# Optimization experiments

Measured on AMD Instinct MI355X. Metric: run time of the kernel, lower is better.

Reference implementation:

```python
import jax, jax.numpy as jnp
import numpy as np

B, N, H = 8, 256, 128
EDGE_IN = 2 * H + 1
NODE_IN = 2 * H


def _glorot(key, shape):
    fan_in, fan_out = shape[0], shape[1]
    lim = 1.0 / np.sqrt(fan_in)
    return jax.random.uniform(key, shape, jnp.float32, -lim, lim)


def setup_inputs() -> dict:
    key = jax.random.key(0)
    ks = jax.random.split(key, 12)
    node_state = jax.random.normal(ks[0], (B, N, H), jnp.float32)
    positions = jax.random.normal(ks[1], (B, N, 3), jnp.float32)
    mask = jnp.ones((B, N), jnp.float32)
    # edge_mlp: Linear(2H+1 -> H), SiLU, Linear(H -> H)  (weights stored [in, out])
    We1 = _glorot(ks[2], (EDGE_IN, H)); be1 = _glorot(ks[3], (1, H))[0]
    We2 = _glorot(ks[4], (H, H));       be2 = _glorot(ks[5], (1, H))[0]
    # node_mlp: Linear(2H -> H), SiLU, Linear(H -> H)
    Wn1 = _glorot(ks[6], (NODE_IN, H)); bn1 = _glorot(ks[7], (1, H))[0]
    Wn2 = _glorot(ks[8], (H, H));       bn2 = _glorot(ks[9], (1, H))[0]
    return {"node_state": node_state, "positions": positions, "mask": mask,
            "We1": We1, "be1": be1, "We2": We2, "be2": be2,
            "Wn1": Wn1, "bn1": bn1, "Wn2": Wn2, "bn2": bn2}


def reference(node_state, positions, mask, We1, be1, We2, be2, Wn1, bn1, Wn2, bn2):
    b, n, h = node_state.shape
    # pairwise distances [B, N, N, 1]; safe-sqrt so grad at i==j is 0 (exact fwd)
    rel = positions[:, :, None, :] - positions[:, None, :, :]
    sq = jnp.sum(rel * rel, axis=-1, keepdims=True)
    dist = jnp.where(sq > 0, jnp.sqrt(jnp.where(sq > 0, sq, 1.0)), 0.0)
    # broadcast-concat node features for all pairs -> [B, N, N, 2H+1]
    node_i = jnp.broadcast_to(node_state[:, :, None, :], (b, n, n, h))
    node_j = jnp.broadcast_to(node_state[:, None, :, :], (b, n, n, h))
    edge_input = jnp.concatenate([node_i, node_j, dist], axis=-1)
    edge_msg = jax.nn.silu(edge_input @ We1 + be1) @ We2 + be2  # [B,N,N,H]
    # pairwise validity mask [B, N, N, 1]
    edge_mask = (mask[:, None, :] * mask[:, :, None])[..., None]
    edge_msg = edge_msg * edge_mask
    # masked mean over j
    denom = jnp.clip(jnp.sum(edge_mask, axis=2), 1.0, None)  # [B,N,1]
    aggregated = jnp.sum(edge_msg, axis=2) / denom           # [B,N,H]
    node_in = jnp.concatenate([node_state, aggregated], axis=-1)
    updated = jax.nn.silu(node_in @ Wn1 + bn1) @ Wn2 + bn2
    return node_state + updated * mask[..., None]
```

## Files before the change

kernel.cpp:

```cpp
#include <hip/hip_runtime.h>
#include <hip/hip_bf16.h>
#include <math.h>

#define B_ 8
#define N_ 256
#define H_ 128
#define NODES_ (B_ * N_)

__device__ __forceinline__ float silu_fast(float x) {
    float e = __expf(-x);
    return x * __builtin_amdgcn_rcpf(1.0f + e);
}

__global__ __launch_bounds__(512) void k1(
    const float* __restrict__ node, const float* __restrict__ We1,
    const float* __restrict__ be1, const float* __restrict__ Wn1,
    const float* __restrict__ bn1, const float* __restrict__ mask,
    float* __restrict__ P, float* __restrict__ Q, float* __restrict__ pre)
{
    __shared__ float act[4][128];
    __shared__ float pls[16][4][128];
    const int t = threadIdx.x;
    const int g = blockIdx.x >> 9;
    const int node0 = (blockIdx.x & 511) * 4;

    if (t < 128) {
        int r = t >> 5, col = (t & 31) * 4;
        *(float4*)(&act[r][col]) = *(const float4*)(node + (size_t)(node0 + r) * H_ + col);
    }
    const float* W = (g == 0) ? We1 : (g == 1) ? (We1 + 128 * H_) : Wn1;
    const int kseg = t >> 5;
    const int c0   = (t & 31) * 4;
    __syncthreads();

    float4 w[8];
    const float* Wb = W + (size_t)(kseg * 8) * H_ + c0;
    #pragma unroll
    for (int u = 0; u < 8; ++u) w[u] = *(const float4*)(Wb + u * H_);

    #pragma unroll
    for (int n = 0; n < 4; ++n) {
        float4 a = {0.f, 0.f, 0.f, 0.f};
        #pragma unroll
        for (int u = 0; u < 8; ++u) {
            float v = act[n][kseg * 8 + u];
            a.x = fmaf(v, w[u].x, a.x);
            a.y = fmaf(v, w[u].y, a.y);
            a.z = fmaf(v, w[u].z, a.z);
            a.w = fmaf(v, w[u].w, a.w);
        }
        *(float4*)(&pls[kseg][n][c0]) = a;
    }
    __syncthreads();

    {
        const int n = t >> 7;
        const int c = t & 127;
        float s = 0.f;
        #pragma unroll
        for (int seg = 0; seg < 16; ++seg) s += pls[seg][n][c];
        float* op;
        if (g == 0)      { op = P;   s += be1[c]; }
        else if (g == 1) { op = Q;   s += (mask[node0 + n] - 1.0f) * 1e30f; }
        else             { op = pre; s += bn1[c]; }
        op[(size_t)(node0 + n) * H_ + c] = s;
    }
}

__global__ __launch_bounds__(512) void k2bc(
    const float* __restrict__ P, const float* __restrict__ Q,
    const float* __restrict__ We1, const float* __restrict__ positions,
    const float* __restrict__ mask, const float* __restrict__ pre,
    const float* __restrict__ node,
    const float* __restrict__ We2, const float* __restrict__ be2,
    const float* __restrict__ Wn1, const float* __restrict__ Wn2,
    const float* __restrict__ bn2, float* __restrict__ out)
{
    __shared__ float arena[8192];
    __shared__ float dls[256][4];
    __shared__ float Sls[4][128];
    __shared__ float Tls[4][128];
    __shared__ float cs;
    const int t  = threadIdx.x;
    const int b  = blockIdx.x >> 6;
    const int i0 = (blockIdx.x & 63) * 4;

    {
        const int t2 = t & 255;
        const int half = t >> 8;
        const int il = t2 & 3;
        const int jb = t2 >> 2;
        const float* pb = positions + b * N_ * 3;
        const float pix = pb[(i0 + il) * 3 + 0];
        const float piy = pb[(i0 + il) * 3 + 1];
        const float piz = pb[(i0 + il) * 3 + 2];
        #pragma unroll
        for (int s = 0; s < 2; ++s) {
            int j = jb + 64 * (half * 2 + s);
            float dx = pix - pb[j * 3 + 0];
            float dy = piy - pb[j * 3 + 1];
            float dz = piz - pb[j * 3 + 2];
            float sq = dx * dx + dy * dy + dz * dz;
            dls[j][il] = (sq > 0.f) ? sqrtf(sq) : 0.f;
        }
    }
    if (t < 64) {
        float mv = mask[b * N_ + t] + mask[b * N_ + 64 + t]
                 + mask[b * N_ + 128 + t] + mask[b * N_ + 192 + t];
        #pragma unroll
        for (int off = 32; off >= 1; off >>= 1) mv += __shfl_down(mv, off);
        if (t == 0) cs = mv;
    }

    const int i = t >> 7;
    const int c = t & 127;
    const float wd   = We1[256 * H_ + c];
    const float base = P[(size_t)(b * N_ + i0 + i) * H_ + c];
    const float4* __restrict__ Qg = (const float4*)(Q + (size_t)(b * N_) * H_);

    float4 r0 = Qg[0 * 512 + t];
    float4 r1 = Qg[1 * 512 + t];
    float4 r2 = Qg[2 * 512 + t];
    float4 r3 = Qg[3 * 512 + t];

    float acc = 0.f;
    for (int ch = 0; ch < 4; ++ch) {
        __syncthreads();
        ((float4*)arena)[0 * 512 + t] = r0;
        ((float4*)arena)[1 * 512 + t] = r1;
        ((float4*)arena)[2 * 512 + t] = r2;
        ((float4*)arena)[3 * 512 + t] = r3;
        if (ch < 3) {
            r0 = Qg[(ch + 1) * 2048 + 0 * 512 + t];
            r1 = Qg[(ch + 1) * 2048 + 1 * 512 + t];
            r2 = Qg[(ch + 1) * 2048 + 2 * 512 + t];
            r3 = Qg[(ch + 1) * 2048 + 3 * 512 + t];
        }
        __syncthreads();
        const int j0 = ch * 64;
        #pragma unroll 8
        for (int jj = 0; jj < 64; ++jj) {
            float q = arena[jj * 128 + c];
            float d = dls[j0 + jj][i];
            float x = fmaf(d, wd, base + q);
            float e = __expf(-x);
            float r = __builtin_amdgcn_rcpf(1.0f + e);
            acc = fmaf(x, r, acc);
        }
    }

    const float inv_cnt = __builtin_amdgcn_rcpf(fmaxf(cs, 1.0f));
    const float mi = mask[b * N_ + i0 + i];
    Sls[i][c] = (mi * inv_cnt) * acc;
    __syncthreads();

    float (*pls)[4][128] = (float (*)[4][128])arena;
    const int kseg = t >> 5;
    const int c0   = (t & 31) * 4;

    {
        const float* Wb = We2 + (size_t)(kseg * 8) * H_ + c0;
        float4 w[8];
        #pragma unroll
        for (int u = 0; u < 8; ++u) w[u] = *(const float4*)(Wb + u * H_);
        #pragma unroll
        for (int n = 0; n < 4; ++n) {
            float4 a = {0.f, 0.f, 0.f, 0.f};
            #pragma unroll
            for (int u = 0; u < 8; ++u) {
                float v = Sls[n][kseg * 8 + u];
                a.x = fmaf(v, w[u].x, a.x); a.y = fmaf(v, w[u].y, a.y);
                a.z = fmaf(v, w[u].z, a.z); a.w = fmaf(v, w[u].w, a.w);
            }
            *(float4*)(&pls[kseg][n][c0]) = a;
        }
    }
    __syncthreads();
    {
        float s = 0.f;
        #pragma unroll
        for (int seg = 0; seg < 16; ++seg) s += pls[seg][i][c];
        Tls[i][c] = fmaf(mi, be2[c], s);
    }
    __syncthreads();

    {
        const float* Wb = Wn1 + (size_t)(128 + kseg * 8) * H_ + c0;
        float4 w[8];
        #pragma unroll
        for (int u = 0; u < 8; ++u) w[u] = *(const float4*)(Wb + u * H_);
        #pragma unroll
        for (int n = 0; n < 4; ++n) {
            float4 a = {0.f, 0.f, 0.f, 0.f};
            #pragma unroll
            for (int u = 0; u < 8; ++u) {
                float v = Tls[n][kseg * 8 + u];
                a.x = fmaf(v, w[u].x, a.x); a.y = fmaf(v, w[u].y, a.y);
                a.z = fmaf(v, w[u].z, a.z); a.w = fmaf(v, w[u].w, a.w);
            }
            *(float4*)(&pls[kseg][n][c0]) = a;
        }
    }
    __syncthreads();
    {
        float s = 0.f;
        #pragma unroll
        for (int seg = 0; seg < 16; ++seg) s += pls[seg][i][c];
        float h = silu_fast(pre[(size_t)(b * N_ + i0 + i) * H_ + c] + s);
        Sls[i][c] = h;
    }
    __syncthreads();

    {
        const float* Wb = Wn2 + (size_t)(kseg * 8) * H_ + c0;
        float4 w[8];
        #pragma unroll
        for (int u = 0; u < 8; ++u) w[u] = *(const float4*)(Wb + u * H_);
        #pragma unroll
        for (int n = 0; n < 4; ++n) {
            float4 a = {0.f, 0.f, 0.f, 0.f};
            #pragma unroll
            for (int u = 0; u < 8; ++u) {
                float v = Sls[n][kseg * 8 + u];
                a.x = fmaf(v, w[u].x, a.x); a.y = fmaf(v, w[u].y, a.y);
                a.z = fmaf(v, w[u].z, a.z); a.w = fmaf(v, w[u].w, a.w);
            }
            *(float4*)(&pls[kseg][n][c0]) = a;
        }
    }
    __syncthreads();
    {
        float s = 0.f;
        #pragma unroll
        for (int seg = 0; seg < 16; ++seg) s += pls[seg][i][c];
        const size_t idx = (size_t)(b * N_ + i0 + i) * H_ + c;
        out[idx] = node[idx] + mi * (s + bn2[c]);
    }
}

extern "C" void kernel_launch(void* const* d_in, const int* in_sizes, int n_in,
                              void* d_out, int out_size, void* d_ws, size_t ws_size,
                              hipStream_t stream)
{
    const float* node      = (const float*)d_in[0];
    const float* positions = (const float*)d_in[1];
    const float* mask      = (const float*)d_in[2];
    const float* We1       = (const float*)d_in[3];
    const float* be1       = (const float*)d_in[4];
    const float* We2       = (const float*)d_in[5];
    const float* be2       = (const float*)d_in[6];
    const float* Wn1       = (const float*)d_in[7];
    const float* bn1       = (const float*)d_in[8];
    const float* Wn2       = (const float*)d_in[9];
    const float* bn2       = (const float*)d_in[10];
    float* out = (float*)d_out;

    const size_t SZ = (size_t)NODES_ * H_;
    float* P   = (float*)d_ws;
    float* Q   = P + SZ;
    float* pre = Q + SZ;

    k1  <<<1536, 512, 0, stream>>>(node, We1, be1, Wn1, bn1, mask, P, Q, pre);
    k2bc<<<512,  512, 0, stream>>>(P, Q, We1, positions, mask, pre, node,
                                   We2, be2, Wn1, Wn2, bn2, out);
}
```

Baseline: 103.4 us.

## Fuse P and pre projections into main kernel, prescale by log2e, vectorize edge loop

The first kernel now computes only the Q projection, writing it prescaled by -log2(e). The P and pre projections move into the second kernel, computed per block in shared memory, which removes two global round-trips and cuts the first launch's grid. The pairwise SiLU loop now has each thread handle four channels over a quarter of the j range, using exp2 directly on prescaled values. Partial sums are reduced through shared memory and the -ln2 factor is applied at the end. The fused kernel does more GEMM work before its main loop and adds extra barriers.

```diff
diff --git a/kernel.cpp b/kernel.cpp
--- a/kernel.cpp
+++ b/kernel.cpp
@@ -1,5 +1,4 @@
 #include <hip/hip_runtime.h>
-#include <hip/hip_bf16.h>
 #include <math.h>
 
 #define B_ 8
@@ -7,83 +6,95 @@
 #define H_ 128
 #define NODES_ (B_ * N_)
 
+#define LOG2E 1.442695041f
+#define LN2   0.6931471806f
+
 __device__ __forceinline__ float silu_fast(float x) {
     float e = __expf(-x);
     return x * __builtin_amdgcn_rcpf(1.0f + e);
 }
 
-__global__ __launch_bounds__(512) void k1(
+__device__ __forceinline__ void splitk_gemm(
+    const float* __restrict__ Wb,
+    const float (*actm)[128],
+    float (*pls)[4][128], int kseg, int c0)
+{
+    float4 w[8];
+    #pragma unroll
+    for (int u = 0; u < 8; ++u) w[u] = *(const float4*)(Wb + u * H_);
+    #pragma unroll
+    for (int n = 0; n < 4; ++n) {
+        float vv[8];
+        *(float4*)(vv)     = *(const float4*)(&actm[n][kseg * 8]);
+        *(float4*)(vv + 4) = *(const float4*)(&actm[n][kseg * 8 + 4]);
+        float4 a = {0.f, 0.f, 0.f, 0.f};
+        #pragma unroll
+        for (int u = 0; u < 8; ++u) {
+            a.x = fmaf(vv[u], w[u].x, a.x);
+            a.y = fmaf(vv[u], w[u].y, a.y);
+            a.z = fmaf(vv[u], w[u].z, a.z);
+            a.w = fmaf(vv[u], w[u].w, a.w);
+        }
+        *(float4*)(&pls[kseg][n][c0]) = a;
+    }
+}
+
+__global__ __launch_bounds__(512) void k1q(
     const float* __restrict__ node, const float* __restrict__ We1,
-    const float* __restrict__ be1, const float* __restrict__ Wn1,
-    const float* __restrict__ bn1, const float* __restrict__ mask,
-    float* __restrict__ P, float* __restrict__ Q, float* __restrict__ pre)
-{
-    __shared__ float act[4][128];
-    __shared__ float pls[16][4][128];
+    const float* __restrict__ mask, float* __restrict__ Q)
+{
+    __shared__ __align__(16) float act[4][128];
+    __shared__ __align__(16) float pls[16][4][128];
     const int t = threadIdx.x;
-    const int g = blockIdx.x >> 9;
-    const int node0 = (blockIdx.x & 511) * 4;
+    const int node0 = blockIdx.x * 4;
 
     if (t < 128) {
         int r = t >> 5, col = (t & 31) * 4;
         *(float4*)(&act[r][col]) = *(const float4*)(node + (size_t)(node0 + r) * H_ + col);
     }
-    const float* W = (g == 0) ? We1 : (g == 1) ? (We1 + 128 * H_) : Wn1;
     const int kseg = t >> 5;
     const int c0   = (t & 31) * 4;
     __syncthreads();
 
-    float4 w[8];
-    const float* Wb = W + (size_t)(kseg * 8) * H_ + c0;
-    #pragma unroll
-    for (int u = 0; u < 8; ++u) w[u] = *(const float4*)(Wb + u * H_);
-
-    #pragma unroll
-    for (int n = 0; n < 4; ++n) {
-        float4 a = {0.f, 0.f, 0.f, 0.f};
-        #pragma unroll
-        for (int u = 0; u < 8; ++u) {
-            float v = act[n][kseg * 8 + u];
-            a.x = fmaf(v, w[u].x, a.x);
-            a.y = fmaf(v, w[u].y, a.y);
-            a.z = fmaf(v, w[u].z, a.z);
-            a.w = fmaf(v, w[u].w, a.w);
-        }
-        *(float4*)(&pls[kseg][n][c0]) = a;
-    }
-    __syncthreads();
-
-    {
-        const int n = t >> 7;
-        const int c = t & 127;
+    splitk_gemm(We1 + (size_t)(128 + kseg * 8) * H_ + c0, act, pls, kseg, c0);
+    __syncthreads();
+    {
+        const int n = t >> 7, c = t & 127;
         float s = 0.f;
         #pragma unroll
         for (int seg = 0; seg < 16; ++seg) s += pls[seg][n][c];
-        float* op;
-        if (g == 0)      { op = P;   s += be1[c]; }
-        else if (g == 1) { op = Q;   s += (mask[node0 + n] - 1.0f) * 1e30f; }
-        else             { op = pre; s += bn1[c]; }
-        op[(size_t)(node0 + n) * H_ + c] = s;
-    }
-}
-
-__global__ __launch_bounds__(512) void k2bc(
-    const float* __restrict__ P, const float* __restrict__ Q,
-    const float* __restrict__ We1, const float* __restrict__ positions,
-    const float* __restrict__ mask, const float* __restrict__ pre,
-    const float* __restrict__ node,
+        const float m = mask[node0 + n];
+        Q[(size_t)(node0 + n) * H_ + c] = fmaf(-LOG2E, s, (1.0f - m) * 1e30f);
+    }
+}
+
+__global__ __launch_bounds__(512) void k2(
+    const float* __restrict__ Qv, const float* __restrict__ We1,
+    const float* __restrict__ be1, const float* __restrict__ positions,
+    const float* __restrict__ mask, const float* __restrict__ node,
     const float* __restrict__ We2, const float* __restrict__ be2,
-    const float* __restrict__ Wn1, const float* __restrict__ Wn2,
-    const float* __restrict__ bn2, float* __restrict__ out)
-{
-    __shared__ float arena[8192];
-    __shared__ float dls[256][4];
-    __shared__ float Sls[4][128];
-    __shared__ float Tls[4][128];
+    const float* __restrict__ Wn1, const float* __restrict__ bn1,
+    const float* __restrict__ Wn2, const float* __restrict__ bn2,
+    float* __restrict__ out)
+{
+    __shared__ __align__(16) float arena[8192];
+    __shared__ __align__(16) float dls[256][4];
+    __shared__ __align__(16) float Sls[4][128];
+    __shared__ __align__(16) float Tls[4][128];
+    __shared__ __align__(16) float Pls[4][128];
+    __shared__ __align__(16) float prels[4][128];
     __shared__ float cs;
+
     const int t  = threadIdx.x;
     const int b  = blockIdx.x >> 6;
     const int i0 = (blockIdx.x & 63) * 4;
+    const int node0 = b * N_ + i0;
+
+    const float4* __restrict__ Qg = (const float4*)(Qv + (size_t)(b * N_) * H_);
+    float4 r0 = Qg[0 * 512 + t];
+    float4 r1 = Qg[1 * 512 + t];
+    float4 r2 = Qg[2 * 512 + t];
+    float4 r3 = Qg[3 * 512 + t];
 
     {
         const int t2 = t & 255;
@@ -112,18 +123,45 @@
         if (t == 0) cs = mv;
     }
 
-    const int i = t >> 7;
-    const int c = t & 127;
-    const float wd   = We1[256 * H_ + c];
-    const float base = P[(size_t)(b * N_ + i0 + i) * H_ + c];
-    const float4* __restrict__ Qg = (const float4*)(Q + (size_t)(b * N_) * H_);
-
-    float4 r0 = Qg[0 * 512 + t];
-    float4 r1 = Qg[1 * 512 + t];
-    float4 r2 = Qg[2 * 512 + t];
-    float4 r3 = Qg[3 * 512 + t];
-
-    float acc = 0.f;
+    const int kseg = t >> 5;
+    const int c0   = (t & 31) * 4;
+    float (*pls)[4][128] = (float (*)[4][128])arena;
+
+    if (t < 128) {
+        int r = t >> 5, col = (t & 31) * 4;
+        *(float4*)(&Tls[r][col]) = *(const float4*)(node + (size_t)(node0 + r) * H_ + col);
+    }
+    __syncthreads();
+    splitk_gemm(We1 + (size_t)(kseg * 8) * H_ + c0, Tls, pls, kseg, c0);
+    __syncthreads();
+    {
+        const int n = t >> 7, c = t & 127;
+        float s = 0.f;
+        #pragma unroll
+        for (int seg = 0; seg < 16; ++seg) s += pls[seg][n][c];
+        Pls[n][c] = -LOG2E * (s + be1[c]);
+    }
+    __syncthreads();
+    splitk_gemm(Wn1 + (size_t)(kseg * 8) * H_ + c0, Tls, pls, kseg, c0);
+    __syncthreads();
+    {
+        const int n = t >> 7, c = t & 127;
+        float s = 0.f;
+        #pragma unroll
+        for (int seg = 0; seg < 16; ++seg) s += pls[seg][n][c];
+        prels[n][c] = s + bn1[c];
+    }
+
+    const int i   = t >> 7;
+    const int jq  = (t >> 5) & 3;
+    const int cg  = t & 31;
+    const int c0e = cg * 4;
+
+    float4 wd4 = *(const float4*)(We1 + (size_t)256 * H_ + c0e);
+    wd4.x *= -LOG2E; wd4.y *= -LOG2E; wd4.z *= -LOG2E; wd4.w *= -LOG2E;
+    const float4 base4 = *(const float4*)(&Pls[i][c0e]);
+    float4 acc = {0.f, 0.f, 0.f, 0.f};
+
     for (int ch = 0; ch < 4; ++ch) {
         __syncthreads();
         ((float4*)arena)[0 * 512 + t] = r0;
@@ -137,46 +175,47 @@
             r3 = Qg[(ch + 1) * 2048 + 3 * 512 + t];
         }
         __syncthreads();
-        const int j0 = ch * 64;
+        const float4* qrow = ((const float4*)arena) + (jq * 16) * 32 + cg;
+        const int jd = ch * 64 + jq * 16;
         #pragma unroll 8
-        for (int jj = 0; jj < 64; ++jj) {
-            float q = arena[jj * 128 + c];
-            float d = dls[j0 + jj][i];
-            float x = fmaf(d, wd, base + q);
-            float e = __expf(-x);
-            float r = __builtin_amdgcn_rcpf(1.0f + e);
-            acc = fmaf(x, r, acc);
-        }
-    }
-
-    const float inv_cnt = __builtin_amdgcn_rcpf(fmaxf(cs, 1.0f));
-    const float mi = mask[b * N_ + i0 + i];
-    Sls[i][c] = (mi * inv_cnt) * acc;
-    __syncthreads();
-
-    float (*pls)[4][128] = (float (*)[4][128])arena;
-    const int kseg = t >> 5;
-    const int c0   = (t & 31) * 4;
-
-    {
-        const float* Wb = We2 + (size_t)(kseg * 8) * H_ + c0;
-        float4 w[8];
-        #pragma unroll
-        for (int u = 0; u < 8; ++u) w[u] = *(const float4*)(Wb + u * H_);
-        #pragma unroll
-        for (int n = 0; n < 4; ++n) {
-            float4 a = {0.f, 0.f, 0.f, 0.f};
-            #pragma unroll
-            for (int u = 0; u < 8; ++u) {
-                float v = Sls[n][kseg * 8 + u];
-                a.x = fmaf(v, w[u].x, a.x); a.y = fmaf(v, w[u].y, a.y);
-                a.z = fmaf(v, w[u].z, a.z); a.w = fmaf(v, w[u].w, a.w);
-            }
-            *(float4*)(&pls[kseg][n][c0]) = a;
-        }
-    }
-    __syncthreads();
-    {
+        for (int jj = 0; jj < 16; ++jj) {
+            float4 q = qrow[jj * 32];
+            float d  = dls[jd + jj][i];
+            float nx = fmaf(d, wd4.x, base4.x + q.x);
+            float ny = fmaf(d, wd4.y, base4.y + q.y);
+            float nz = fmaf(d, wd4.z, base4.z + q.z);
+            float nw = fmaf(d, wd4.w, base4.w + q.w);
+            float ex = __builtin_amdgcn_exp2f(nx);
+            float ey = __builtin_amdgcn_exp2f(ny);
+            float ez = __builtin_amdgcn_exp2f(nz);
+            float ew = __builtin_amdgcn_exp2f(nw);
+            acc.x = fmaf(nx, __builtin_amdgcn_rcpf(1.0f + ex), acc.x);
+            acc.y = fmaf(ny, __builtin_amdgcn_rcpf(1.0f + ey), acc.y);
+            acc.z = fmaf(nz, __builtin_amdgcn_rcpf(1.0f + ez), acc.z);
+            acc.w = fmaf(nw, __builtin_amdgcn_rcpf(1.0f + ew), acc.w);
+        }
+    }
+
+    __syncthreads();
+    {
+        float (*pq)[4][128] = (float (*)[4][128])arena;
+        *(float4*)(&pq[jq][i][c0e]) = acc;
+    }
+    __syncthreads();
+    const float mi = mask[node0 + i];
+    {
+        const int c = t & 127;
+        float (*pq)[4][128] = (float (*)[4][128])arena;
+        float s = pq[0][i][c] + pq[1][i][c] + pq[2][i][c] + pq[3][i][c];
+        const float inv_cnt = __builtin_amdgcn_rcpf(fmaxf(cs, 1.0f));
+        Sls[i][c] = (mi * inv_cnt * -LN2) * s;
+    }
+    __syncthreads();
+
+    splitk_gemm(We2 + (size_t)(kseg * 8) * H_ + c0, Sls, pls, kseg, c0);
+    __syncthreads();
+    {
+        const int c = t & 127;
         float s = 0.f;
         #pragma unroll
         for (int seg = 0; seg < 16; ++seg) s += pls[seg][i][c];
@@ -184,56 +223,25 @@
     }
     __syncthreads();
 
-    {
-        const float* Wb = Wn1 + (size_t)(128 + kseg * 8) * H_ + c0;
-        float4 w[8];
-        #pragma unroll
-        for (int u = 0; u < 8; ++u) w[u] = *(const float4*)(Wb + u * H_);
-        #pragma unroll
-        for (int n = 0; n < 4; ++n) {
-            float4 a = {0.f, 0.f, 0.f, 0.f};
-            #pragma unroll
-            for (int u = 0; u < 8; ++u) {
-                float v = Tls[n][kseg * 8 + u];
-                a.x = fmaf(v, w[u].x, a.x); a.y = fmaf(v, w[u].y, a.y);
-                a.z = fmaf(v, w[u].z, a.z); a.w = fmaf(v, w[u].w, a.w);
-            }
-            *(float4*)(&pls[kseg][n][c0]) = a;
-        }
-    }
-    __syncthreads();
-    {
+    splitk_gemm(Wn1 + (size_t)(128 + kseg * 8) * H_ + c0, Tls, pls, kseg, c0);
+    __syncthreads();
+    {
+        const int c = t & 127;
         float s = 0.f;
         #pragma unroll
         for (int seg = 0; seg < 16; ++seg) s += pls[seg][i][c];
-        float h = silu_fast(pre[(size_t)(b * N_ + i0 + i) * H_ + c] + s);
-        Sls[i][c] = h;
-    }
-    __syncthreads();
-
-    {
-        const float* Wb = Wn2 + (size_t)(kseg * 8) * H_ + c0;
-        float4 w[8];
-        #pragma unroll
-        for (int u = 0; u < 8; ++u) w[u] = *(const float4*)(Wb + u * H_);
-        #pragma unroll
-        for (int n = 0; n < 4; ++n) {
-            float4 a = {0.f, 0.f, 0.f, 0.f};
-            #pragma unroll
-            for (int u = 0; u < 8; ++u) {
-                float v = Sls[n][kseg * 8 + u];
-                a.x = fmaf(v, w[u].x, a.x); a.y = fmaf(v, w[u].y, a.y);
-                a.z = fmaf(v, w[u].z, a.z); a.w = fmaf(v, w[u].w, a.w);
-            }
-            *(float4*)(&pls[kseg][n][c0]) = a;
-        }
-    }
-    __syncthreads();
-    {
+        Sls[i][c] = silu_fast(prels[i][c] + s);
+    }
+    __syncthreads();
+
+    splitk_gemm(Wn2 + (size_t)(kseg * 8) * H_ + c0, Sls, pls, kseg, c0);
+    __syncthreads();
+    {
+        const int c = t & 127;
         float s = 0.f;
         #pragma unroll
         for (int seg = 0; seg < 16; ++seg) s += pls[seg][i][c];
-        const size_t idx = (size_t)(b * N_ + i0 + i) * H_ + c;
+        const size_t idx = (size_t)(node0 + i) * H_ + c;
         out[idx] = node[idx] + mi * (s + bn2[c]);
     }
 }
@@ -255,12 +263,9 @@
     const float* bn2       = (const float*)d_in[10];
     float* out = (float*)d_out;
 
-    const size_t SZ = (size_t)NODES_ * H_;
-    float* P   = (float*)d_ws;
-    float* Q   = P + SZ;
-    float* pre = Q + SZ;
-
-    k1  <<<1536, 512, 0, stream>>>(node, We1, be1, Wn1, bn1, mask, P, Q, pre);
-    k2bc<<<512,  512, 0, stream>>>(P, Q, We1, positions, mask, pre, node,
-                                   We2, be2, Wn1, Wn2, bn2, out);
-}
+    float* Q = (float*)d_ws;
+
+    k1q<<<512, 512, 0, stream>>>(node, We1, mask, Q);
+    k2 <<<512, 512, 0, stream>>>(Q, We1, be1, positions, mask, node,
+                                 We2, be2, Wn1, bn1, Wn2, bn2, out);
+}
```

Measured after the change: 101.4 us. About the same (-1.9%).
